# Kernel tuning notes

Hardware: AMD Instinct MI355X
Metric: run time of the kernel (lower is better)

The kernel has to match this reference:

```python
import jax, jax.numpy as jnp
import numpy as np

N, E, D, B = 50000, 800000, 64, 64
NEXP, NC, EDIM, PDIM = 4, 10, 4, 100


def setup_inputs() -> dict:
    key = jax.random.key(0)
    ks = jax.random.split(key, 24)
    s = lambda f: 1.0 / np.sqrt(f)
    inp = {
        'x': jax.random.normal(ks[0], (N, D), jnp.float32),
        'edge_index': jax.random.randint(ks[1], (2, E), 0, N, jnp.int32),
        'edge_attr': jax.random.normal(ks[2], (E, EDIM), jnp.float32),
        'batch': jnp.sort(jax.random.randint(ks[3], (N,), 0, B, jnp.int32)),
        'ldxb_flag': jax.random.normal(ks[4], (B,), jnp.float32),
        # layer 1 params
        'w_edge1': jax.random.normal(ks[5], (D, EDIM)) * s(EDIM),
        'b_edge1': jnp.zeros((D,), jnp.float32),
        'w_ih1': jax.random.normal(ks[6], (3 * D, D)) * s(D),
        'w_hh1': jax.random.normal(ks[7], (3 * D, D)) * s(D),
        'b_ih1': jnp.zeros((3 * D,), jnp.float32),
        'b_hh1': jnp.zeros((3 * D,), jnp.float32),
        # layer 2 params
        'w_edge2': jax.random.normal(ks[8], (D, EDIM)) * s(EDIM),
        'b_edge2': jnp.zeros((D,), jnp.float32),
        'w_ih2': jax.random.normal(ks[9], (3 * D, D)) * s(D),
        'w_hh2': jax.random.normal(ks[10], (3 * D, D)) * s(D),
        'b_ih2': jnp.zeros((3 * D,), jnp.float32),
        'b_hh2': jnp.zeros((3 * D,), jnp.float32),
        # MoE
        'gate_w': jax.random.normal(ks[11], (NEXP, D)) * s(D),
        'gate_b': jnp.zeros((NEXP,), jnp.float32),
        'exp_w': jax.random.normal(ks[12], (NEXP, D, D)) * s(D),
        'exp_b': jnp.zeros((NEXP, D), jnp.float32),
        # heads
        'proj_w': jax.random.normal(ks[13], (PDIM, 1)),
        'proj_b': jnp.zeros((PDIM,), jnp.float32),
        'fc_w': jax.random.normal(ks[14], (NC, D + PDIM)) * s(D + PDIM),
        'fc_b': jnp.zeros((NC,), jnp.float32),
    }
    return inp


def _ggnn_layer(x, src, dst, eemb, w_ih, w_hh, b_ih, b_hh):
    # gather + scatter-add message passing (self-loops already in src/dst/eemb)
    msg = x[src] + eemb                       # [E+N, D]
    m = jnp.zeros_like(x).at[dst].add(msg)    # [N, D]
    # GRUCell(m, x): x is the hidden state
    gi = m @ w_ih.T + b_ih
    gh = x @ w_hh.T + b_hh
    i_r, i_z, i_n = jnp.split(gi, 3, axis=1)
    h_r, h_z, h_n = jnp.split(gh, 3, axis=1)
    r = jax.nn.sigmoid(i_r + h_r)
    z = jax.nn.sigmoid(i_z + h_z)
    n = jnp.tanh(i_n + r * h_n)
    return (1.0 - z) * n + z * x


def reference(x, edge_index, edge_attr, batch, ldxb_flag,
              w_edge1, b_edge1, w_ih1, w_hh1, b_ih1, b_hh1,
              w_edge2, b_edge2, w_ih2, w_hh2, b_ih2, b_hh2,
              gate_w, gate_b, exp_w, exp_b, proj_w, proj_b, fc_w, fc_b):
    n = x.shape[0]
    loop = jnp.arange(n, dtype=edge_index.dtype)
    src = jnp.concatenate([edge_index[0], loop])
    dst = jnp.concatenate([edge_index[1], loop])
    ea = jnp.concatenate([edge_attr, jnp.zeros((n, edge_attr.shape[1]), edge_attr.dtype)], axis=0)

    h = _ggnn_layer(x, src, dst, ea @ w_edge1.T + b_edge1, w_ih1, w_hh1, b_ih1, b_hh1)
    h = jax.nn.relu(h)
    h = _ggnn_layer(h, src, dst, ea @ w_edge2.T + b_edge2, w_ih2, w_hh2, b_ih2, b_hh2)
    h = jax.nn.relu(h)

    # soft MoE combine
    gw = jax.nn.softmax(h @ gate_w.T + gate_b, axis=1)            # [N, NEXP]
    eo = jax.nn.relu(jnp.einsum('nd,ehd->neh', h, exp_w) + exp_b)  # [N, NEXP, D]
    h = jnp.einsum('ne,neh->nh', gw, eo)                           # [N, D]

    # global mean pool per graph
    sums = jax.ops.segment_sum(h, batch, num_segments=B)
    cnts = jax.ops.segment_sum(jnp.ones((n,), h.dtype), batch, num_segments=B)
    graph_emb = sums / jnp.maximum(cnts, 1.0)[:, None]             # [B, D]

    flag = ldxb_flag[:, None] @ proj_w.T + proj_b                  # [B, 100]
    logits = jnp.concatenate([flag, graph_emb], axis=1) @ fc_w.T + fc_b
    return (graph_emb, graph_emb, logits)
```

## Files before the change

kernel.cpp:

```cpp
#include <hip/hip_runtime.h>
#include <hip/hip_fp16.h>
#include <stdint.h>


#define SLOTS 64
#define OVF_MAX 32768
#define PS 16

typedef __bf16 bf16x8 __attribute__((ext_vector_type(8)));
typedef float floatx4 __attribute__((ext_vector_type(4)));
typedef unsigned short us8 __attribute__((ext_vector_type(8)));

__device__ __forceinline__ unsigned short f2bf(float f){
  union { float f; unsigned u; } c; c.f = f;
  unsigned r = c.u + 0x7FFFu + ((c.u >> 16) & 1u);
  return (unsigned short)(r >> 16);
}
__device__ __forceinline__ float bf2f(unsigned short u){
  union { unsigned u; float f; } c; c.u = ((unsigned)u) << 16; return c.f;
}
__device__ __forceinline__ unsigned short f2h(float f){
  return __half_as_ushort(__float2half(f));
}
__device__ __forceinline__ float h2f(unsigned short u){
  return __half2float(__ushort_as_half(u));
}
__device__ __forceinline__ float sigm(float x){ return 1.f/(1.f + __expf(-x)); }

__global__ void k_init(const float* __restrict__ s0, const float* __restrict__ s1,
                       const float* __restrict__ s2, const float* __restrict__ s3,
                       const float* __restrict__ s4, const float* __restrict__ s5,
                       unsigned short* __restrict__ dst,
                       int* __restrict__ cur, int* __restrict__ ovfcnt, int Ncur,
                       const float* __restrict__ xin, unsigned short* __restrict__ x16,
                       int nTot){
  int i = blockIdx.x*blockDim.x + threadIdx.x;
  if (i < Ncur) cur[i] = 0;
  if (i == 0){ ovfcnt[0] = 0; }
  int base = i*8;
  if (base < nTot){
    const float4* xp = (const float4*)(xin + base);
    float4 a = xp[0], b = xp[1];
    us8 t;
    t[0]=f2h(a.x); t[1]=f2h(a.y); t[2]=f2h(a.z); t[3]=f2h(a.w);
    t[4]=f2h(b.x); t[5]=f2h(b.y); t[6]=f2h(b.z); t[7]=f2h(b.w);
    *(us8*)(x16 + base) = t;
  }
  if (i >= 65792) return;
  const float* s; int off;
  if      (i < 12288){ s = s0; off = i; }
  else if (i < 24576){ s = s1; off = i - 12288; }
  else if (i < 36864){ s = s2; off = i - 24576; }
  else if (i < 49152){ s = s3; off = i - 36864; }
  else if (i < 49408){ s = s4; off = i - 49152; }
  else               { s = s5; off = i - 49408; }
  dst[i] = f2bf(s[off]);
}

__global__ void k_bucket(const int* __restrict__ ei, const float* __restrict__ ea,
                         int* __restrict__ cur, int4* __restrict__ bkt,
                         int* __restrict__ ovfcnt, int* __restrict__ ovf,
                         int E, int N){
  int base = blockIdx.x*512;
#pragma unroll
  for (int half = 0; half < 2; ++half){
    int e = base + half*256 + threadIdx.x;
    if (e >= E) continue;
    int s = ei[e];
    int d = ei[E + e];
    int pos = atomicAdd(&cur[d], 1);
    if (pos < SLOTS){
      float4 v = *(const float4*)(ea + (size_t)e*4);
      int4 p;
      p.x = s;
      p.y = (int)(((unsigned)f2bf(v.y) << 16) | (unsigned)f2bf(v.x));
      p.z = (int)(((unsigned)f2bf(v.w) << 16) | (unsigned)f2bf(v.z));
      p.w = 0;
      bkt[(size_t)d*SLOTS + pos] = p;
    } else {
      int o = atomicAdd(ovfcnt, 1);
      if (o < OVF_MAX) ovf[o] = e;
    }
  }
}

#define GATHER8(MM, SRC, A)                                                \
  {                                                                        \
    unsigned long long m2 = (MM);                                          \
    if (m2){                                                               \
      int l0=(int)__builtin_ctzll(m2); m2 &= m2-1;                         \
      A[0] = h2f(x16[(size_t)__shfl((SRC), l0)*64 + d]);                   \
      if (m2){                                                             \
        int l1=(int)__builtin_ctzll(m2); m2 &= m2-1;                       \
        A[1] = h2f(x16[(size_t)__shfl((SRC), l1)*64 + d]);                 \
        if (m2){                                                           \
          int l2=(int)__builtin_ctzll(m2); m2 &= m2-1;                     \
          A[2] = h2f(x16[(size_t)__shfl((SRC), l2)*64 + d]);               \
          if (m2){                                                         \
            int l3=(int)__builtin_ctzll(m2); m2 &= m2-1;                   \
            A[3] = h2f(x16[(size_t)__shfl((SRC), l3)*64 + d]);             \
            if (m2){                                                       \
              int l4=(int)__builtin_ctzll(m2); m2 &= m2-1;                 \
              A[4] = h2f(x16[(size_t)__shfl((SRC), l4)*64 + d]);           \
              if (m2){                                                     \
                int l5=(int)__builtin_ctzll(m2); m2 &= m2-1;               \
                A[5] = h2f(x16[(size_t)__shfl((SRC), l5)*64 + d]);         \
                if (m2){                                                   \
                  int l6=(int)__builtin_ctzll(m2); m2 &= m2-1;             \
                  A[6] = h2f(x16[(size_t)__shfl((SRC), l6)*64 + d]);       \
                  if (m2){                                                 \
                    int l7=(int)__builtin_ctzll(m2); m2 &= m2-1;           \
                    A[7] = h2f(x16[(size_t)__shfl((SRC), l7)*64 + d]);     \
                  }                                                        \
                }                                                          \
              }                                                            \
            }                                                              \
          }                                                                \
        }                                                                  \
      }                                                                    \
    }                                                                      \
    (MM) = m2;                                                             \
  }

__device__ __forceinline__ void gather4_ovf(
    const int* __restrict__ cur, const int4* __restrict__ bkt,
    const float* __restrict__ xin, const unsigned short* __restrict__ x16,
    const float* __restrict__ w_edge, const float* __restrict__ b_edge,
    const int* __restrict__ ei, const float* __restrict__ ea,
    const int* __restrict__ ovf, int cnt, int E,
    float (*mt)[68], int tile, int w, int lane, int N){
  int d = lane;
  float4 wv = *(const float4*)(w_edge + d*4);
  float be = b_edge[d];
  int n0 = tile*16 + w*4;

  int nc[4]; int myc[4]; float selfv[4];
#pragma unroll
  for (int nl = 0; nl < 4; ++nl){
    int n = n0 + nl;
    nc[nl] = n < N ? n : N-1;
    myc[nl] = cur[nc[nl]];
    selfv[nl] = xin[(size_t)nc[nl]*64 + d];
  }
  bool valid[4]; int4 ps[4];
#pragma unroll
  for (int nl = 0; nl < 4; ++nl){
    int vmin = myc[nl] < SLOTS ? myc[nl] : SLOTS;
    valid[nl] = d < vmin;
    int4 z; z.x = 0; z.y = 0; z.z = 0; z.w = 0;
    ps[nl] = valid[nl] ? bkt[(size_t)nc[nl]*SLOTS + d] : z;
  }
  unsigned long long mm[4]; int src[4];
#pragma unroll
  for (int nl = 0; nl < 4; ++nl){
    int vmin = myc[nl] < SLOTS ? myc[nl] : SLOTS;
    mm[nl] = (vmin >= 64) ? ~0ULL : ((1ULL << vmin) - 1ULL);
    src[nl] = ps[nl].x;
  }
  float acc[4];
#pragma unroll
  for (int nl = 0; nl < 4; ++nl) acc[nl] = 0.f;
  while (mm[0] | mm[1] | mm[2] | mm[3]){
    float a[4][8];
#pragma unroll
    for (int nl = 0; nl < 4; ++nl){
#pragma unroll
      for (int jj = 0; jj < 8; ++jj) a[nl][jj] = 0.f;
      GATHER8(mm[nl], src[nl], a[nl]);
    }
#pragma unroll
    for (int nl = 0; nl < 4; ++nl)
      acc[nl] += ((a[nl][0]+a[nl][1])+(a[nl][2]+a[nl][3]))
               + ((a[nl][4]+a[nl][5])+(a[nl][6]+a[nl][7]));
  }
#pragma unroll
  for (int nl = 0; nl < 4; ++nl){
    float ex = 0.f, ey = 0.f, ez = 0.f, ew = 0.f;
    if (valid[nl]){
      ex = bf2f((unsigned short)(ps[nl].y & 0xffff));
      ey = bf2f((unsigned short)(((unsigned)ps[nl].y) >> 16));
      ez = bf2f((unsigned short)(ps[nl].z & 0xffff));
      ew = bf2f((unsigned short)(((unsigned)ps[nl].z) >> 16));
    }
#pragma unroll
    for (int off = 1; off < 64; off <<= 1){
      ex += __shfl_xor(ex, off);
      ey += __shfl_xor(ey, off);
      ez += __shfl_xor(ez, off);
      ew += __shfl_xor(ew, off);
    }
    mt[w*4 + nl][d] = selfv[nl] + (float)(myc[nl] + 1) * be + acc[nl]
                    + ex*wv.x + ey*wv.y + ez*wv.z + ew*wv.w;
  }
  int lo = tile*16;
  for (int base = 0; base < cnt; base += 64){
    int idx = base + lane;
    int eid = (idx < cnt) ? ovf[idx] : -1;
    int dst = (eid >= 0) ? ei[(size_t)E + eid] : -1;
    int rel = dst - lo;
    bool hit = (eid >= 0) && (rel >= 0) && (rel < 16) && ((rel >> 2) == w);
    unsigned long long hm = __ballot(hit);
    while (hm){
      int l = (int)__builtin_ctzll(hm); hm &= hm - 1;
      int e2 = __shfl(eid, l);
      int r2 = __shfl(rel, l);
      int s2 = ei[e2];
      float4 v = *(const float4*)(ea + (size_t)e2*4);
      float addv = xin[(size_t)s2*64 + d] + v.x*wv.x + v.y*wv.y + v.z*wv.z + v.w*wv.w;
      mt[r2][d] += addv;
    }
  }
}

__device__ __forceinline__ void gru3(
    const float (*mt)[68], const float* __restrict__ x,
    const unsigned short* __restrict__ wih, const unsigned short* __restrict__ whh,
    int tile, int j, int col, int quad, int N,
    floatx4* ai, floatx4* ah){
  int na = tile*16 + col; if (na > N-1) na = N-1;
  bf16x8 am[2], ax[2];
#pragma unroll
  for (int ks = 0; ks < 2; ++ks){
    int kb = ks*32 + quad*8;
    const float* mrow = &mt[col][kb];
    float4 lo = *(const float4*)mrow, hi = *(const float4*)(mrow + 4);
    us8 tm;
    tm[0]=f2bf(lo.x); tm[1]=f2bf(lo.y); tm[2]=f2bf(lo.z); tm[3]=f2bf(lo.w);
    tm[4]=f2bf(hi.x); tm[5]=f2bf(hi.y); tm[6]=f2bf(hi.z); tm[7]=f2bf(hi.w);
    am[ks] = __builtin_bit_cast(bf16x8, tm);
    const float4* xp = (const float4*)(x + (size_t)na*64 + kb);
    float4 xlo = xp[0], xhi = xp[1];
    us8 tx;
    tx[0]=f2bf(xlo.x); tx[1]=f2bf(xlo.y); tx[2]=f2bf(xlo.z); tx[3]=f2bf(xlo.w);
    tx[4]=f2bf(xhi.x); tx[5]=f2bf(xhi.y); tx[6]=f2bf(xhi.z); tx[7]=f2bf(xhi.w);
    ax[ks] = __builtin_bit_cast(bf16x8, tx);
  }
#pragma unroll
  for (int g = 0; g < 3; ++g){ ai[g] = (floatx4)0.f; ah[g] = (floatx4)0.f; }
#pragma unroll
  for (int g = 0; g < 3; ++g){
    int r = (g*4 + j)*16 + col;
#pragma unroll
    for (int ks = 0; ks < 2; ++ks){
      int kb = ks*32 + quad*8;
      bf16x8 bi = __builtin_bit_cast(bf16x8, *(const us8*)(wih + (size_t)r*64 + kb));
      ai[g] = __builtin_amdgcn_mfma_f32_16x16x32_bf16(am[ks], bi, ai[g], 0,0,0);
      bf16x8 bh = __builtin_bit_cast(bf16x8, *(const us8*)(whh + (size_t)r*64 + kb));
      ah[g] = __builtin_amdgcn_mfma_f32_16x16x32_bf16(ax[ks], bh, ah[g], 0,0,0);
    }
  }
}

__global__ void __launch_bounds__(256) k_fused1(
    const int* __restrict__ cur, const int4* __restrict__ bkt,
    const float* __restrict__ x, const unsigned short* __restrict__ x16,
    const float* __restrict__ w_edge, const float* __restrict__ b_edge,
    const int* __restrict__ ei, const float* __restrict__ ea,
    const int* __restrict__ ovf, const int* __restrict__ ovfcnt, int E,
    const unsigned short* __restrict__ wih, const unsigned short* __restrict__ whh,
    const float* __restrict__ b_ih, const float* __restrict__ b_hh,
    float* __restrict__ hout, unsigned short* __restrict__ h16out,
    int tiles, int N){
  __shared__ __align__(16) float mt[16][68];
  int tile = blockIdx.x; if (tile >= tiles) return;
  int w = threadIdx.x >> 6, lane = threadIdx.x & 63;
  int cnt = *ovfcnt; if (cnt > OVF_MAX) cnt = OVF_MAX;
  gather4_ovf(cur, bkt, x, x16, w_edge, b_edge, ei, ea, ovf, cnt, E,
              mt, tile, w, lane, N);
  __syncthreads();

  int col = lane & 15, quad = lane >> 4, j = w;
  floatx4 ai[3], ah[3];
  gru3(mt, x, wih, whh, tile, j, col, quad, N, ai, ah);

  int dd = j*16 + col;
  float bir = b_ih[dd],      bhr = b_hh[dd];
  float biz = b_ih[64+dd],   bhz = b_hh[64+dd];
  float bin = b_ih[128+dd],  bhn = b_hh[128+dd];
#pragma unroll
  for (int rg = 0; rg < 4; ++rg){
    int node = tile*16 + quad*4 + rg;
    if (node >= N) continue;
    float rr = sigm(ai[0][rg] + bir + ah[0][rg] + bhr);
    float zz = sigm(ai[1][rg] + biz + ah[1][rg] + bhz);
    float nn = tanhf(ai[2][rg] + bin + rr*(ah[2][rg] + bhn));
    float xv = x[(size_t)node*64 + dd];
    float hv = fmaxf((1.f - zz)*nn + zz*xv, 0.f);
    hout[(size_t)node*64 + dd] = hv;
    h16out[(size_t)node*64 + dd] = f2h(hv);
  }
}

__global__ void __launch_bounds__(256) k_fused2(
    const int* __restrict__ cur, const int4* __restrict__ bkt,
    const float* __restrict__ h, const unsigned short* __restrict__ h16,
    const float* __restrict__ w_edge, const float* __restrict__ b_edge,
    const int* __restrict__ ei, const float* __restrict__ ea,
    const int* __restrict__ ovf, const int* __restrict__ ovfcnt, int E,
    const unsigned short* __restrict__ wih, const unsigned short* __restrict__ whh,
    const float* __restrict__ b_ih, const float* __restrict__ b_hh,
    const unsigned short* __restrict__ gate_w, const float* __restrict__ gate_b,
    const unsigned short* __restrict__ exp_w,  const float* __restrict__ exp_b,
    float* __restrict__ v_out, int tiles, int N){
  __shared__ __align__(16) float mt[16][68];
  __shared__ __align__(16) unsigned short ht16s[1024];
  __shared__ float gsm[16][4];
  __shared__ float vsm[4][16][65];
  int tile = blockIdx.x; if (tile >= tiles) return;
  int w = threadIdx.x >> 6, lane = threadIdx.x & 63;
  int cnt = *ovfcnt; if (cnt > OVF_MAX) cnt = OVF_MAX;
  gather4_ovf(cur, bkt, h, h16, w_edge, b_edge, ei, ea, ovf, cnt, E,
              mt, tile, w, lane, N);
  __syncthreads();

  int col = lane & 15, quad = lane >> 4, j = w;
  floatx4 ai[3], ah[3];
  gru3(mt, h, wih, whh, tile, j, col, quad, N, ai, ah);

  int dd = j*16 + col;
  {
    float bir = b_ih[dd],      bhr = b_hh[dd];
    float biz = b_ih[64+dd],   bhz = b_hh[64+dd];
    float bin = b_ih[128+dd],  bhn = b_hh[128+dd];
#pragma unroll
    for (int rg = 0; rg < 4; ++rg){
      int nloc = quad*4 + rg;
      int node = tile*16 + nloc;
      int na2 = node < N ? node : N-1;
      float rr = sigm(ai[0][rg] + bir + ah[0][rg] + bhr);
      float zz = sigm(ai[1][rg] + biz + ah[1][rg] + bhz);
      float nn = tanhf(ai[2][rg] + bin + rr*(ah[2][rg] + bhn));
      float xv = h[(size_t)na2*64 + dd];
      float hv = fmaxf((1.f - zz)*nn + zz*xv, 0.f);
      int addr = (nloc*128 + dd*2) ^ ((nloc & 7) << 4);
      *(unsigned short*)((char*)ht16s + addr) = f2bf(hv);
    }
  }
  __syncthreads();

  bf16x8 a2[2];
#pragma unroll
  for (int ks = 0; ks < 2; ++ks){
    int badd = (col*128 + ks*64 + quad*16) ^ ((col & 7) << 4);
    a2[ks] = __builtin_bit_cast(bf16x8, *(const us8*)((const char*)ht16s + badd));
  }
  if (j == 0){
    floatx4 accg = (floatx4)0.f;
#pragma unroll
    for (int ks = 0; ks < 2; ++ks){
      int kb = ks*32 + quad*8;
      us8 braw = {0,0,0,0,0,0,0,0};
      if (col < 4) braw = *(const us8*)(gate_w + col*64 + kb);
      accg = __builtin_amdgcn_mfma_f32_16x16x32_bf16(a2[ks], __builtin_bit_cast(bf16x8, braw), accg, 0,0,0);
    }
    if (col < 4){
      float gb = gate_b[col];
#pragma unroll
      for (int rg = 0; rg < 4; ++rg) gsm[quad*4+rg][col] = accg[rg] + gb;
    }
  }
  floatx4 acc2[4];
#pragma unroll
  for (int nt = 0; nt < 4; ++nt) acc2[nt] = (floatx4)0.f;
#pragma unroll
  for (int nt = 0; nt < 4; ++nt)
#pragma unroll
    for (int ks = 0; ks < 2; ++ks){
      int kb = ks*32 + quad*8;
      bf16x8 b = __builtin_bit_cast(bf16x8,
          *(const us8*)(exp_w + ((size_t)j*64 + nt*16 + col)*64 + kb));
      acc2[nt] = __builtin_amdgcn_mfma_f32_16x16x32_bf16(a2[ks], b, acc2[nt], 0,0,0);
    }
  __syncthreads();

#pragma unroll
  for (int rg = 0; rg < 4; ++rg){
    int nrow = quad*4 + rg;
    float g0=gsm[nrow][0], g1=gsm[nrow][1], g2=gsm[nrow][2], g3=gsm[nrow][3];
    float mx = fmaxf(fmaxf(g0,g1), fmaxf(g2,g3));
    float e0=__expf(g0-mx), e1=__expf(g1-mx), e2=__expf(g2-mx), e3=__expf(g3-mx);
    float we = ((j==0)?e0:(j==1)?e1:(j==2)?e2:e3) / (e0+e1+e2+e3);
#pragma unroll
    for (int nt = 0; nt < 4; ++nt){
      int o = nt*16 + col;
      vsm[j][nrow][o] = we * fmaxf(acc2[nt][rg] + exp_b[j*64 + o], 0.f);
    }
  }
  __syncthreads();

  for (int idx = threadIdx.x; idx < 1024; idx += 256){
    int nrow = idx >> 6, o = idx & 63;
    int node = tile*16 + nrow;
    if (node < N)
      v_out[(size_t)node*64 + o] = vsm[0][nrow][o] + vsm[1][nrow][o]
                                 + vsm[2][nrow][o] + vsm[3][nrow][o];
  }
}

__device__ __forceinline__ int lower_bound_i(const int* __restrict__ a, int n, int key){
  int lo = 0, hi = n;
  while (lo < hi){ int mid = (lo + hi) >> 1; if (a[mid] < key) lo = mid + 1; else hi = mid; }
  return lo;
}

__global__ void __launch_bounds__(256) k_pool(
    const float* __restrict__ v, const int* __restrict__ batch, int N,
    float* __restrict__ partial){
  __shared__ float red[4][64];
  int g = blockIdx.x / PS, s = blockIdx.x % PS;
  int t = threadIdx.x, d = t & 63, r = t >> 6;
  int start = lower_bound_i(batch, N, g);
  int end   = lower_bound_i(batch, N, g + 1);
  int len = end - start;
  int per = (len + PS - 1) / PS;
  int s0 = start + s*per;
  int s1 = s0 + per; if (s1 > end) s1 = end;
  float acc = 0.f;
  for (int i = s0 + r; i < s1; i += 4)
    acc += v[(size_t)i*64 + d];
  red[r][d] = acc;
  __syncthreads();
  if (r == 0)
    partial[(size_t)blockIdx.x*64 + d] = red[0][d] + red[1][d] + red[2][d] + red[3][d];
}

__global__ void __launch_bounds__(64) k_head(
    const float* __restrict__ partial, const int* __restrict__ batch, int N, int B,
    const float* __restrict__ ldxb,
    const float* __restrict__ proj_w, const float* __restrict__ proj_b,
    const float* __restrict__ fc_w, const float* __restrict__ fc_b,
    float* __restrict__ out){
  __shared__ float ges[64];
  int b = blockIdx.x, d = threadIdx.x;
  int start = lower_bound_i(batch, N, b);
  int end   = lower_bound_i(batch, N, b + 1);
  float sum = 0.f;
#pragma unroll
  for (int s = 0; s < PS; ++s)
    sum += partial[((size_t)b*PS + s)*64 + d];
  float ge = sum / fmaxf((float)(end - start), 1.f);
  ges[d] = ge;
  out[(size_t)b*64 + d]                = ge;
  out[(size_t)B*64 + (size_t)b*64 + d] = ge;
  __syncthreads();
  if (d < 10){
    float acc = fc_b[d];
    float fl = ldxb[b];
    const float* fr = fc_w + d*164;
    for (int p = 0; p < 100; ++p) acc += (fl*proj_w[p] + proj_b[p]) * fr[p];
    for (int dd = 0; dd < 64; ++dd) acc += ges[dd]*fr[100 + dd];
    out[(size_t)B*128 + (size_t)b*10 + d] = acc;
  }
}

extern "C" void kernel_launch(void* const* d_in, const int* in_sizes, int n_in,
                              void* d_out, int out_size, void* d_ws, size_t ws_size,
                              hipStream_t stream){
  const float* x      = (const float*)d_in[0];
  const int*   ei     = (const int*)d_in[1];
  const float* ea     = (const float*)d_in[2];
  const int*   batch  = (const int*)d_in[3];
  const float* ldxb   = (const float*)d_in[4];
  const float* w_edge1= (const float*)d_in[5];
  const float* b_edge1= (const float*)d_in[6];
  const float* w_ih1  = (const float*)d_in[7];
  const float* w_hh1  = (const float*)d_in[8];
  const float* b_ih1  = (const float*)d_in[9];
  const float* b_hh1  = (const float*)d_in[10];
  const float* w_edge2= (const float*)d_in[11];
  const float* b_edge2= (const float*)d_in[12];
  const float* w_ih2  = (const float*)d_in[13];
  const float* w_hh2  = (const float*)d_in[14];
  const float* b_ih2  = (const float*)d_in[15];
  const float* b_hh2  = (const float*)d_in[16];
  const float* gate_w = (const float*)d_in[17];
  const float* gate_b = (const float*)d_in[18];
  const float* exp_w  = (const float*)d_in[19];
  const float* exp_b  = (const float*)d_in[20];
  const float* proj_w = (const float*)d_in[21];
  const float* proj_b = (const float*)d_in[22];
  const float* fc_w   = (const float*)d_in[23];
  const float* fc_b   = (const float*)d_in[24];
  float* out = (float*)d_out;

  int N = in_sizes[0] / 64;
  int E = in_sizes[1] / 2;
  int B = in_sizes[4];
  int tiles = (N + 15) / 16;
  int nTot = N * 64;

  float*   v       = (float*)d_ws;
  float*   h       = v + (size_t)nTot;
  int4*    bkt     = (int4*)(h + (size_t)nTot);
  int*     cur     = (int*)(bkt + (size_t)nTot);
  int*     ovfcnt  = cur + (size_t)N*8;
  int*     ovf     = ovfcnt + 4;
  unsigned short* wbf = (unsigned short*)(ovf + OVF_MAX);
  float*   partial = (float*)(wbf + 65792);
  unsigned short* x16 = (unsigned short*)(partial + (size_t)B*PS*64);
  unsigned short* h16 = x16 + (size_t)nTot;
  unsigned short* wih1bf = wbf;
  unsigned short* whh1bf = wbf + 12288;
  unsigned short* wih2bf = wbf + 24576;
  unsigned short* whh2bf = wbf + 36864;
  unsigned short* gatebf = wbf + 49152;
  unsigned short* expbf  = wbf + 49408;

  dim3 blk(256);
  int edgeBlocks = (E + 511)/512;
  int initThreads = N > 65792 ? N : 65792;
  if (nTot/8 > initThreads) initThreads = nTot/8;
  int initBlocks = (initThreads + 255)/256;

  k_init<<<initBlocks, blk, 0, stream>>>(w_ih1, w_hh1, w_ih2, w_hh2, gate_w, exp_w,
                                         wbf, cur, ovfcnt, N, x, x16, nTot);
  k_bucket<<<edgeBlocks, blk, 0, stream>>>(ei, ea, cur, bkt, ovfcnt, ovf, E, N);
  k_fused1<<<tiles, blk, 0, stream>>>(cur, bkt, x, x16, w_edge1, b_edge1,
                                      ei, ea, ovf, ovfcnt, E,
                                      wih1bf, whh1bf, b_ih1, b_hh1,
                                      h, h16, tiles, N);
  k_fused2<<<tiles, blk, 0, stream>>>(cur, bkt, h, h16, w_edge2, b_edge2,
                                      ei, ea, ovf, ovfcnt, E,
                                      wih2bf, whh2bf, b_ih2, b_hh2,
                                      gatebf, gate_b, expbf, exp_b,
                                      v, tiles, N);
  k_pool<<<B*PS, blk, 0, stream>>>(v, batch, N, partial);
  k_head<<<B, 64, 0, stream>>>(partial, batch, N, B, ldxb, proj_w, proj_b, fc_w, fc_b, out);
}
```

Baseline: 343.4 us.

## Use half/bf16 node features throughout, scalar-lane gather loop, fast sigmoid/tanh

Drops the fp32 hidden-state buffer. Node features are kept as fp16 copies for gathering and bf16 copies for the MFMA GRU inputs, and the message tile is staged in LDS as bf16. This removes fp32 loads and per-use conversions. The bitmask/ctz gather becomes a wave-uniform loop that reads source indices with readlane, and overflow edges now accumulate in registers instead of LDS. Sigmoid, tanh and the softmax divide switch to hardware reciprocal approximations, and expert outputs are staged in fp16. This lowers precision of self-values and intermediates.

Result: slower. 354.7 us (+3.3%).

```diff
diff --git a/kernel.cpp b/kernel.cpp
--- a/kernel.cpp
+++ b/kernel.cpp
@@ -25,15 +25,21 @@
 __device__ __forceinline__ float h2f(unsigned short u){
   return __half2float(__ushort_as_half(u));
 }
-__device__ __forceinline__ float sigm(float x){ return 1.f/(1.f + __expf(-x)); }
+__device__ __forceinline__ float sigm(float x){
+  return __builtin_amdgcn_rcpf(1.f + __expf(-x));
+}
+__device__ __forceinline__ float ftanh(float x){
+  return 1.f - 2.f*__builtin_amdgcn_rcpf(__expf(2.f*x) + 1.f);
+}
 
 __global__ void k_init(const float* __restrict__ s0, const float* __restrict__ s1,
                        const float* __restrict__ s2, const float* __restrict__ s3,
                        const float* __restrict__ s4, const float* __restrict__ s5,
                        unsigned short* __restrict__ dst,
                        int* __restrict__ cur, int* __restrict__ ovfcnt, int Ncur,
-                       const float* __restrict__ xin, unsigned short* __restrict__ x16,
-                       int nTot){
+                       const float* __restrict__ xin,
+                       unsigned short* __restrict__ x16,
+                       unsigned short* __restrict__ xb, int nTot){
   int i = blockIdx.x*blockDim.x + threadIdx.x;
   if (i < Ncur) cur[i] = 0;
   if (i == 0){ ovfcnt[0] = 0; }
@@ -41,10 +47,13 @@
   if (base < nTot){
     const float4* xp = (const float4*)(xin + base);
     float4 a = xp[0], b = xp[1];
-    us8 t;
-    t[0]=f2h(a.x); t[1]=f2h(a.y); t[2]=f2h(a.z); t[3]=f2h(a.w);
-    t[4]=f2h(b.x); t[5]=f2h(b.y); t[6]=f2h(b.z); t[7]=f2h(b.w);
-    *(us8*)(x16 + base) = t;
+    us8 t16, tb;
+    t16[0]=f2h(a.x); t16[1]=f2h(a.y); t16[2]=f2h(a.z); t16[3]=f2h(a.w);
+    t16[4]=f2h(b.x); t16[5]=f2h(b.y); t16[6]=f2h(b.z); t16[7]=f2h(b.w);
+    tb[0]=f2bf(a.x); tb[1]=f2bf(a.y); tb[2]=f2bf(a.z); tb[3]=f2bf(a.w);
+    tb[4]=f2bf(b.x); tb[5]=f2bf(b.y); tb[6]=f2bf(b.z); tb[7]=f2bf(b.w);
+    *(us8*)(x16 + base) = t16;
+    *(us8*)(xb + base) = tb;
   }
   if (i >= 65792) return;
   const float* s; int off;
@@ -84,51 +93,13 @@
   }
 }
 
-#define GATHER8(MM, SRC, A)                                                \
-  {                                                                        \
-    unsigned long long m2 = (MM);                                          \
-    if (m2){                                                               \
-      int l0=(int)__builtin_ctzll(m2); m2 &= m2-1;                         \
-      A[0] = h2f(x16[(size_t)__shfl((SRC), l0)*64 + d]);                   \
-      if (m2){                                                             \
-        int l1=(int)__builtin_ctzll(m2); m2 &= m2-1;                       \
-        A[1] = h2f(x16[(size_t)__shfl((SRC), l1)*64 + d]);                 \
-        if (m2){                                                           \
-          int l2=(int)__builtin_ctzll(m2); m2 &= m2-1;                     \
-          A[2] = h2f(x16[(size_t)__shfl((SRC), l2)*64 + d]);               \
-          if (m2){                                                         \
-            int l3=(int)__builtin_ctzll(m2); m2 &= m2-1;                   \
-            A[3] = h2f(x16[(size_t)__shfl((SRC), l3)*64 + d]);             \
-            if (m2){                                                       \
-              int l4=(int)__builtin_ctzll(m2); m2 &= m2-1;                 \
-              A[4] = h2f(x16[(size_t)__shfl((SRC), l4)*64 + d]);           \
-              if (m2){                                                     \
-                int l5=(int)__builtin_ctzll(m2); m2 &= m2-1;               \
-                A[5] = h2f(x16[(size_t)__shfl((SRC), l5)*64 + d]);         \
-                if (m2){                                                   \
-                  int l6=(int)__builtin_ctzll(m2); m2 &= m2-1;             \
-                  A[6] = h2f(x16[(size_t)__shfl((SRC), l6)*64 + d]);       \
-                  if (m2){                                                 \
-                    int l7=(int)__builtin_ctzll(m2); m2 &= m2-1;           \
-                    A[7] = h2f(x16[(size_t)__shfl((SRC), l7)*64 + d]);     \
-                  }                                                        \
-                }                                                          \
-              }                                                            \
-            }                                                              \
-          }                                                                \
-        }                                                                  \
-      }                                                                    \
-    }                                                                      \
-    (MM) = m2;                                                             \
-  }
-
 __device__ __forceinline__ void gather4_ovf(
     const int* __restrict__ cur, const int4* __restrict__ bkt,
-    const float* __restrict__ xin, const unsigned short* __restrict__ x16,
+    const unsigned short* __restrict__ x16,
     const float* __restrict__ w_edge, const float* __restrict__ b_edge,
     const int* __restrict__ ei, const float* __restrict__ ea,
     const int* __restrict__ ovf, int cnt, int E,
-    float (*mt)[68], int tile, int w, int lane, int N){
+    unsigned short (*mt16)[72], int tile, int w, int lane, int N){
   int d = lane;
   float4 wv = *(const float4*)(w_edge + d*4);
   float be = b_edge[d];
@@ -140,7 +111,7 @@
     int n = n0 + nl;
     nc[nl] = n < N ? n : N-1;
     myc[nl] = cur[nc[nl]];
-    selfv[nl] = xin[(size_t)nc[nl]*64 + d];
+    selfv[nl] = h2f(x16[(size_t)nc[nl]*64 + d]);
   }
   bool valid[4]; int4 ps[4];
 #pragma unroll
@@ -150,51 +121,40 @@
     int4 z; z.x = 0; z.y = 0; z.z = 0; z.w = 0;
     ps[nl] = valid[nl] ? bkt[(size_t)nc[nl]*SLOTS + d] : z;
   }
-  unsigned long long mm[4]; int src[4];
+  int src[4];
+#pragma unroll
+  for (int nl = 0; nl < 4; ++nl) src[nl] = ps[nl].x;
+
+  float acc[4];
+#pragma unroll
+  for (int nl = 0; nl < 4; ++nl) acc[nl] = 0.f;
 #pragma unroll
   for (int nl = 0; nl < 4; ++nl){
-    int vmin = myc[nl] < SLOTS ? myc[nl] : SLOTS;
-    mm[nl] = (vmin >= 64) ? ~0ULL : ((1ULL << vmin) - 1ULL);
-    src[nl] = ps[nl].x;
-  }
-  float acc[4];
-#pragma unroll
-  for (int nl = 0; nl < 4; ++nl) acc[nl] = 0.f;
-  while (mm[0] | mm[1] | mm[2] | mm[3]){
-    float a[4][8];
-#pragma unroll
-    for (int nl = 0; nl < 4; ++nl){
-#pragma unroll
-      for (int jj = 0; jj < 8; ++jj) a[nl][jj] = 0.f;
-      GATHER8(mm[nl], src[nl], a[nl]);
-    }
-#pragma unroll
-    for (int nl = 0; nl < 4; ++nl)
-      acc[nl] += ((a[nl][0]+a[nl][1])+(a[nl][2]+a[nl][3]))
-               + ((a[nl][4]+a[nl][5])+(a[nl][6]+a[nl][7]));
-  }
-#pragma unroll
-  for (int nl = 0; nl < 4; ++nl){
-    float ex = 0.f, ey = 0.f, ez = 0.f, ew = 0.f;
-    if (valid[nl]){
-      ex = bf2f((unsigned short)(ps[nl].y & 0xffff));
-      ey = bf2f((unsigned short)(((unsigned)ps[nl].y) >> 16));
-      ez = bf2f((unsigned short)(ps[nl].z & 0xffff));
-      ew = bf2f((unsigned short)(((unsigned)ps[nl].z) >> 16));
-    }
-#pragma unroll
-    for (int off = 1; off < 64; off <<= 1){
-      ex += __shfl_xor(ex, off);
-      ey += __shfl_xor(ey, off);
-      ez += __shfl_xor(ez, off);
-      ew += __shfl_xor(ew, off);
-    }
-    mt[w*4 + nl][d] = selfv[nl] + (float)(myc[nl] + 1) * be + acc[nl]
-                    + ex*wv.x + ey*wv.y + ez*wv.z + ew*wv.w;
+    int m = __builtin_amdgcn_readfirstlane(myc[nl] < SLOTS ? myc[nl] : SLOTS);
+    for (int r = 0; r < m; r += 8){
+      float a0=0.f,a1=0.f,a2=0.f,a3=0.f,a4=0.f,a5=0.f,a6=0.f,a7=0.f;
+      { int ss = __builtin_amdgcn_readlane(src[nl], r);
+        a0 = h2f(x16[(size_t)ss*64 + d]); }
+      if (r+1 < m){ int ss = __builtin_amdgcn_readlane(src[nl], r+1);
+        a1 = h2f(x16[(size_t)ss*64 + d]); }
+      if (r+2 < m){ int ss = __builtin_amdgcn_readlane(src[nl], r+2);
+        a2 = h2f(x16[(size_t)ss*64 + d]); }
+      if (r+3 < m){ int ss = __builtin_amdgcn_readlane(src[nl], r+3);
+        a3 = h2f(x16[(size_t)ss*64 + d]); }
+      if (r+4 < m){ int ss = __builtin_amdgcn_readlane(src[nl], r+4);
+        a4 = h2f(x16[(size_t)ss*64 + d]); }
+      if (r+5 < m){ int ss = __builtin_amdgcn_readlane(src[nl], r+5);
+        a5 = h2f(x16[(size_t)ss*64 + d]); }
+      if (r+6 < m){ int ss = __builtin_amdgcn_readlane(src[nl], r+6);
+        a6 = h2f(x16[(size_t)ss*64 + d]); }
+      if (r+7 < m){ int ss = __builtin_amdgcn_readlane(src[nl], r+7);
+        a7 = h2f(x16[(size_t)ss*64 + d]); }
+      acc[nl] += ((a0 + a1) + (a2 + a3)) + ((a4 + a5) + (a6 + a7));
+    }
   }
   int lo = tile*16;
-  for (int base = 0; base < cnt; base += 64){
-    int idx = base + lane;
+  for (int base2 = 0; base2 < cnt; base2 += 64){
+    int idx = base2 + lane;
     int eid = (idx < cnt) ? ovf[idx] : -1;
     int dst = (eid >= 0) ? ei[(size_t)E + eid] : -1;
     int rel = dst - lo;
@@ -205,15 +165,40 @@
       int e2 = __shfl(eid, l);
       int r2 = __shfl(rel, l);
       int s2 = ei[e2];
-      float4 v = *(const float4*)(ea + (size_t)e2*4);
-      float addv = xin[(size_t)s2*64 + d] + v.x*wv.x + v.y*wv.y + v.z*wv.z + v.w*wv.w;
-      mt[r2][d] += addv;
-    }
+      float4 vv = *(const float4*)(ea + (size_t)e2*4);
+      float addv = h2f(x16[(size_t)s2*64 + d])
+                 + vv.x*wv.x + vv.y*wv.y + vv.z*wv.z + vv.w*wv.w;
+      int t = r2 & 3;
+      acc[0] += (t==0) ? addv : 0.f;
+      acc[1] += (t==1) ? addv : 0.f;
+      acc[2] += (t==2) ? addv : 0.f;
+      acc[3] += (t==3) ? addv : 0.f;
+    }
+  }
+#pragma unroll
+  for (int nl = 0; nl < 4; ++nl){
+    float ex = 0.f, ey = 0.f, ez = 0.f, ew = 0.f;
+    if (valid[nl]){
+      ex = bf2f((unsigned short)(ps[nl].y & 0xffff));
+      ey = bf2f((unsigned short)(((unsigned)ps[nl].y) >> 16));
+      ez = bf2f((unsigned short)(ps[nl].z & 0xffff));
+      ew = bf2f((unsigned short)(((unsigned)ps[nl].z) >> 16));
+    }
+#pragma unroll
+    for (int off = 1; off < 64; off <<= 1){
+      ex += __shfl_xor(ex, off);
+      ey += __shfl_xor(ey, off);
+      ez += __shfl_xor(ez, off);
+      ew += __shfl_xor(ew, off);
+    }
+    float val = selfv[nl] + (float)(myc[nl] + 1) * be + acc[nl]
+              + ex*wv.x + ey*wv.y + ez*wv.z + ew*wv.w;
+    mt16[w*4 + nl][d] = f2bf(val);
   }
 }
 
 __device__ __forceinline__ void gru3(
-    const float (*mt)[68], const float* __restrict__ x,
+    const unsigned short (*mt16)[72], const unsigned short* __restrict__ xb,
     const unsigned short* __restrict__ wih, const unsigned short* __restrict__ whh,
     int tile, int j, int col, int quad, int N,
     floatx4* ai, floatx4* ah){
@@ -222,18 +207,8 @@
 #pragma unroll
   for (int ks = 0; ks < 2; ++ks){
     int kb = ks*32 + quad*8;
-    const float* mrow = &mt[col][kb];
-    float4 lo = *(const float4*)mrow, hi = *(const float4*)(mrow + 4);
-    us8 tm;
-    tm[0]=f2bf(lo.x); tm[1]=f2bf(lo.y); tm[2]=f2bf(lo.z); tm[3]=f2bf(lo.w);
-    tm[4]=f2bf(hi.x); tm[5]=f2bf(hi.y); tm[6]=f2bf(hi.z); tm[7]=f2bf(hi.w);
-    am[ks] = __builtin_bit_cast(bf16x8, tm);
-    const float4* xp = (const float4*)(x + (size_t)na*64 + kb);
-    float4 xlo = xp[0], xhi = xp[1];
-    us8 tx;
-    tx[0]=f2bf(xlo.x); tx[1]=f2bf(xlo.y); tx[2]=f2bf(xlo.z); tx[3]=f2bf(xlo.w);
-    tx[4]=f2bf(xhi.x); tx[5]=f2bf(xhi.y); tx[6]=f2bf(xhi.z); tx[7]=f2bf(xhi.w);
-    ax[ks] = __builtin_bit_cast(bf16x8, tx);
+    am[ks] = __builtin_bit_cast(bf16x8, *(const us8*)&mt16[col][kb]);
+    ax[ks] = __builtin_bit_cast(bf16x8, *(const us8*)(xb + (size_t)na*64 + kb));
   }
 #pragma unroll
   for (int g = 0; g < 3; ++g){ ai[g] = (floatx4)0.f; ah[g] = (floatx4)0.f; }
@@ -253,25 +228,25 @@
 
 __global__ void __launch_bounds__(256) k_fused1(
     const int* __restrict__ cur, const int4* __restrict__ bkt,
-    const float* __restrict__ x, const unsigned short* __restrict__ x16,
+    const unsigned short* __restrict__ x16, const unsigned short* __restrict__ xb,
     const float* __restrict__ w_edge, const float* __restrict__ b_edge,
     const int* __restrict__ ei, const float* __restrict__ ea,
     const int* __restrict__ ovf, const int* __restrict__ ovfcnt, int E,
     const unsigned short* __restrict__ wih, const unsigned short* __restrict__ whh,
     const float* __restrict__ b_ih, const float* __restrict__ b_hh,
-    float* __restrict__ hout, unsigned short* __restrict__ h16out,
+    unsigned short* __restrict__ h16out, unsigned short* __restrict__ hbout,
     int tiles, int N){
-  __shared__ __align__(16) float mt[16][68];
+  __shared__ __align__(16) unsigned short mt16[16][72];
   int tile = blockIdx.x; if (tile >= tiles) return;
   int w = threadIdx.x >> 6, lane = threadIdx.x & 63;
   int cnt = *ovfcnt; if (cnt > OVF_MAX) cnt = OVF_MAX;
-  gather4_ovf(cur, bkt, x, x16, w_edge, b_edge, ei, ea, ovf, cnt, E,
-              mt, tile, w, lane, N);
+  gather4_ovf(cur, bkt, x16, w_edge, b_edge, ei, ea, ovf, cnt, E,
+              mt16, tile, w, lane, N);
   __syncthreads();
 
   int col = lane & 15, quad = lane >> 4, j = w;
   floatx4 ai[3], ah[3];
-  gru3(mt, x, wih, whh, tile, j, col, quad, N, ai, ah);
+  gru3(mt16, xb, wih, whh, tile, j, col, quad, N, ai, ah);
 
   int dd = j*16 + col;
   float bir = b_ih[dd],      bhr = b_hh[dd];
@@ -283,17 +258,17 @@
     if (node >= N) continue;
     float rr = sigm(ai[0][rg] + bir + ah[0][rg] + bhr);
     float zz = sigm(ai[1][rg] + biz + ah[1][rg] + bhz);
-    float nn = tanhf(ai[2][rg] + bin + rr*(ah[2][rg] + bhn));
-    float xv = x[(size_t)node*64 + dd];
+    float nn = ftanh(ai[2][rg] + bin + rr*(ah[2][rg] + bhn));
+    float xv = h2f(x16[(size_t)node*64 + dd]);
     float hv = fmaxf((1.f - zz)*nn + zz*xv, 0.f);
-    hout[(size_t)node*64 + dd] = hv;
     h16out[(size_t)node*64 + dd] = f2h(hv);
+    hbout [(size_t)node*64 + dd] = f2bf(hv);
   }
 }
 
 __global__ void __launch_bounds__(256) k_fused2(
     const int* __restrict__ cur, const int4* __restrict__ bkt,
-    const float* __restrict__ h, const unsigned short* __restrict__ h16,
+    const unsigned short* __restrict__ h16, const unsigned short* __restrict__ hb,
     const float* __restrict__ w_edge, const float* __restrict__ b_edge,
     const int* __restrict__ ei, const float* __restrict__ ea,
     const int* __restrict__ ovf, const int* __restrict__ ovfcnt, int E,
@@ -302,20 +277,20 @@
     const unsigned short* __restrict__ gate_w, const float* __restrict__ gate_b,
     const unsigned short* __restrict__ exp_w,  const float* __restrict__ exp_b,
     float* __restrict__ v_out, int tiles, int N){
-  __shared__ __align__(16) float mt[16][68];
+  __shared__ __align__(16) unsigned short mt16[16][72];
   __shared__ __align__(16) unsigned short ht16s[1024];
   __shared__ float gsm[16][4];
-  __shared__ float vsm[4][16][65];
+  __shared__ unsigned short vsm16[4][16][65];
   int tile = blockIdx.x; if (tile >= tiles) return;
   int w = threadIdx.x >> 6, lane = threadIdx.x & 63;
   int cnt = *ovfcnt; if (cnt > OVF_MAX) cnt = OVF_MAX;
-  gather4_ovf(cur, bkt, h, h16, w_edge, b_edge, ei, ea, ovf, cnt, E,
-              mt, tile, w, lane, N);
+  gather4_ovf(cur, bkt, h16, w_edge, b_edge, ei, ea, ovf, cnt, E,
+              mt16, tile, w, lane, N);
   __syncthreads();
 
   int col = lane & 15, quad = lane >> 4, j = w;
   floatx4 ai[3], ah[3];
-  gru3(mt, h, wih, whh, tile, j, col, quad, N, ai, ah);
+  gru3(mt16, hb, wih, whh, tile, j, col, quad, N, ai, ah);
 
   int dd = j*16 + col;
   {
@@ -329,8 +304,8 @@
       int na2 = node < N ? node : N-1;
       float rr = sigm(ai[0][rg] + bir + ah[0][rg] + bhr);
       float zz = sigm(ai[1][rg] + biz + ah[1][rg] + bhz);
-      float nn = tanhf(ai[2][rg] + bin + rr*(ah[2][rg] + bhn));
-      float xv = h[(size_t)na2*64 + dd];
+      float nn = ftanh(ai[2][rg] + bin + rr*(ah[2][rg] + bhn));
+      float xv = h2f(h16[(size_t)na2*64 + dd]);
       float hv = fmaxf((1.f - zz)*nn + zz*xv, 0.f);
       int addr = (nloc*128 + dd*2) ^ ((nloc & 7) << 4);
       *(unsigned short*)((char*)ht16s + addr) = f2bf(hv);
@@ -379,11 +354,12 @@
     float g0=gsm[nrow][0], g1=gsm[nrow][1], g2=gsm[nrow][2], g3=gsm[nrow][3];
     float mx = fmaxf(fmaxf(g0,g1), fmaxf(g2,g3));
     float e0=__expf(g0-mx), e1=__expf(g1-mx), e2=__expf(g2-mx), e3=__expf(g3-mx);
-    float we = ((j==0)?e0:(j==1)?e1:(j==2)?e2:e3) / (e0+e1+e2+e3);
+    float inv = __builtin_amdgcn_rcpf(e0+e1+e2+e3);
+    float we = ((j==0)?e0:(j==1)?e1:(j==2)?e2:e3) * inv;
 #pragma unroll
     for (int nt = 0; nt < 4; ++nt){
       int o = nt*16 + col;
-      vsm[j][nrow][o] = we * fmaxf(acc2[nt][rg] + exp_b[j*64 + o], 0.f);
+      vsm16[j][nrow][o] = f2h(we * fmaxf(acc2[nt][rg] + exp_b[j*64 + o], 0.f));
     }
   }
   __syncthreads();
@@ -392,8 +368,8 @@
     int nrow = idx >> 6, o = idx & 63;
     int node = tile*16 + nrow;
     if (node < N)
-      v_out[(size_t)node*64 + o] = vsm[0][nrow][o] + vsm[1][nrow][o]
-                                 + vsm[2][nrow][o] + vsm[3][nrow][o];
+      v_out[(size_t)node*64 + o] = h2f(vsm16[0][nrow][o]) + h2f(vsm16[1][nrow][o])
+                                 + h2f(vsm16[2][nrow][o]) + h2f(vsm16[3][nrow][o]);
   }
 }
 
@@ -490,8 +466,9 @@
   int nTot = N * 64;
 
   float*   v       = (float*)d_ws;
-  float*   h       = v + (size_t)nTot;
-  int4*    bkt     = (int4*)(h + (size_t)nTot);
+  unsigned short* xb = (unsigned short*)(v + (size_t)nTot);
+  unsigned short* hb = xb + (size_t)nTot;
+  int4*    bkt     = (int4*)(hb + (size_t)nTot);
   int*     cur     = (int*)(bkt + (size_t)nTot);
   int*     ovfcnt  = cur + (size_t)N*8;
   int*     ovf     = ovfcnt + 4;
@@ -513,13 +490,13 @@
   int initBlocks = (initThreads + 255)/256;
 
   k_init<<<initBlocks, blk, 0, stream>>>(w_ih1, w_hh1, w_ih2, w_hh2, gate_w, exp_w,
-                                         wbf, cur, ovfcnt, N, x, x16, nTot);
+                                         wbf, cur, ovfcnt, N, x, x16, xb, nTot);
   k_bucket<<<edgeBlocks, blk, 0, stream>>>(ei, ea, cur, bkt, ovfcnt, ovf, E, N);
-  k_fused1<<<tiles, blk, 0, stream>>>(cur, bkt, x, x16, w_edge1, b_edge1,
+  k_fused1<<<tiles, blk, 0, stream>>>(cur, bkt, x16, xb, w_edge1, b_edge1,
                                       ei, ea, ovf, ovfcnt, E,
                                       wih1bf, whh1bf, b_ih1, b_hh1,
-                                      h, h16, tiles, N);
-  k_fused2<<<tiles, blk, 0, stream>>>(cur, bkt, h, h16, w_edge2, b_edge2,
+                                      h16, hb, tiles, N);
+  k_fused2<<<tiles, blk, 0, stream>>>(cur, bkt, h16, hb, w_edge2, b_edge2,
                                       ei, ea, ovf, ovfcnt, E,
                                       wih2bf, whh2bf, b_ih2, b_hh2,
                                       gatebf, gate_b, expbf, exp_b,
```
